# Optimization experiments

Hardware: AMD Instinct MI355X
Metric: run time of the kernel (lower is better)

The kernel has to match this reference:

```python
import jax, jax.numpy as jnp
import numpy as np

B, S, H, NH = 2, 2048, 1024, 16
HD = H // NH  # 64
EPS = 1e-5


def setup_inputs() -> dict:
    key = jax.random.key(0)
    ks = jax.random.split(key, 4)
    return {
        "hidden_states": jax.random.normal(ks[0], (B, S, H), dtype=jnp.float32),
        "W_attn": jax.random.normal(ks[1], (H, 3 * H), dtype=jnp.float32) * (1.0 / np.sqrt(H)),
        "b_attn": jnp.zeros((3 * H,), dtype=jnp.float32),
        "W_proj": jax.random.normal(ks[2], (H, H), dtype=jnp.float32) * (1.0 / np.sqrt(H)),
        "b_proj": jnp.zeros((H,), dtype=jnp.float32),
        "q_gamma": jnp.ones((HD,), dtype=jnp.float32),
        "q_beta": jnp.zeros((HD,), dtype=jnp.float32),
        "k_gamma": jnp.ones((HD,), dtype=jnp.float32),
        "k_beta": jnp.zeros((HD,), dtype=jnp.float32),
    }


def _layernorm(x, gamma, beta):
    mu = jnp.mean(x, axis=-1, keepdims=True)
    var = jnp.mean(jnp.square(x - mu), axis=-1, keepdims=True)
    return (x - mu) * jax.lax.rsqrt(var + EPS) * gamma + beta


def reference(hidden_states, W_attn, b_attn, W_proj, b_proj, q_gamma, q_beta, k_gamma, k_beta):
    b, s, h = hidden_states.shape
    qkv = hidden_states @ W_attn + b_attn  # [B,S,3H]
    q, k, v = jnp.split(qkv, 3, axis=-1)
    # [B,S,H] -> [B,NH,S,HD]
    def to_heads(t):
        return t.reshape(b, s, NH, HD).transpose(0, 2, 1, 3)
    q, k, v = to_heads(q), to_heads(k), to_heads(v)
    # QK LayerNorm over head_dim
    q = _layernorm(q, q_gamma, q_beta)
    k = _layernorm(k, k_gamma, k_beta)
    scale = HD ** (-0.5)
    scores = jnp.einsum("bhqd,bhkd->bhqk", q, k) * scale
    causal = jnp.tril(jnp.ones((s, s), dtype=bool))
    mask_value = jnp.finfo(scores.dtype).min
    scores = jnp.where(causal, scores, mask_value)
    attn = jax.nn.softmax(scores.astype(jnp.float32), axis=-1).astype(q.dtype)
    out = jnp.einsum("bhqk,bhkd->bhqd", attn, v)
    out = out.transpose(0, 2, 1, 3).reshape(b, s, h)
    out = out @ W_proj + b_proj
    return out
```

## Files before the change

### kernel.cpp

```cpp
#include <hip/hip_runtime.h>
#include <hip/hip_bf16.h>

typedef __bf16 bf16x8 __attribute__((ext_vector_type(8)));
typedef float f32x4 __attribute__((ext_vector_type(4)));

#define EPS 1e-5f
#define QSCALE 0.18033688011112042f

__device__ __forceinline__ unsigned short f2bf(float f) {
  union { float f; unsigned int i; } c; c.f = f;
  unsigned int r = c.i + 0x7FFFu + ((c.i >> 16) & 1u);
  return (unsigned short)(r >> 16);
}
__device__ __forceinline__ unsigned short f2bf_t(float f) {
  union { float f; unsigned int i; } c; c.f = f;
  return (unsigned short)(c.i >> 16);
}

__device__ __forceinline__ void glds16(const void* g, void* l) {
  __builtin_amdgcn_global_load_lds(
      (const __attribute__((address_space(1))) unsigned int*)g,
      (__attribute__((address_space(3))) unsigned int*)l, 16, 0, 0);
}

__device__ __forceinline__ void transpose_tile(
    const float* __restrict__ in, unsigned short* __restrict__ out,
    int R, int C, int ct0, int rt0, unsigned short* S )
{
  const int t = threadIdx.x;
  const int r = t >> 2, c4 = (t & 3) * 16;
  {
    long base = (long)(rt0 + r) * C + ct0 + c4;
    float4 a = *(const float4*)&in[base];
    float4 b = *(const float4*)&in[base + 4];
    float4 c = *(const float4*)&in[base + 8];
    float4 d = *(const float4*)&in[base + 12];
    unsigned short v[16] = {f2bf(a.x), f2bf(a.y), f2bf(a.z), f2bf(a.w),
                            f2bf(b.x), f2bf(b.y), f2bf(b.z), f2bf(b.w),
                            f2bf(c.x), f2bf(c.y), f2bf(c.z), f2bf(c.w),
                            f2bf(d.x), f2bf(d.y), f2bf(d.z), f2bf(d.w)};
    *(uint4*)&S[r * 72 + c4]     = *(uint4*)&v[0];
    *(uint4*)&S[r * 72 + c4 + 8] = *(uint4*)&v[8];
  }
  __syncthreads();
  unsigned short tmp[16];
#pragma unroll
  for (int j = 0; j < 16; j++) tmp[j] = S[(c4 + j) * 72 + r];
  *(uint4*)&out[(long)(ct0 + r) * R + rt0 + c4]     = *(uint4*)&tmp[0];
  *(uint4*)&out[(long)(ct0 + r) * R + rt0 + c4 + 8] = *(uint4*)&tmp[8];
}

__global__ __launch_bounds__(256) void prep_kernel(
    const float* __restrict__ Wa, const float* __restrict__ Wp,
    const float* __restrict__ X,
    unsigned short* __restrict__ WaT, unsigned short* __restrict__ WpT,
    unsigned short* __restrict__ Xbf)
{
  __shared__ __align__(16) unsigned short S[64 * 72];
  const int id = blockIdx.x;
  if (id < 768) {
    transpose_tile(Wa, WaT, 1024, 3072, (id % 48) * 64, (id / 48) * 64, S);
  } else if (id < 1024) {
    const int i2 = id - 768;
    transpose_tile(Wp, WpT, 1024, 1024, (i2 % 16) * 64, (i2 / 16) * 64, S);
  } else {
    long i = ((long)(id - 1024) * 256 + threadIdx.x) * 16;
    float4 a = *(const float4*)&X[i];
    float4 b = *(const float4*)&X[i + 4];
    float4 c = *(const float4*)&X[i + 8];
    float4 d = *(const float4*)&X[i + 12];
    unsigned short v[16] = {f2bf(a.x), f2bf(a.y), f2bf(a.z), f2bf(a.w),
                            f2bf(b.x), f2bf(b.y), f2bf(b.z), f2bf(b.w),
                            f2bf(c.x), f2bf(c.y), f2bf(c.z), f2bf(c.w),
                            f2bf(d.x), f2bf(d.y), f2bf(d.z), f2bf(d.w)};
    *(uint4*)&Xbf[i]     = *(uint4*)&v[0];
    *(uint4*)&Xbf[i + 8] = *(uint4*)&v[8];
  }
}

__global__ __launch_bounds__(256) void qkvt_kernel(
    const float* __restrict__ Xf,
    const unsigned short* __restrict__ Xbf, int use_xbf,
    const unsigned short* __restrict__ WT,
    const float* __restrict__ bias,
    const float* __restrict__ qg, const float* __restrict__ qb,
    const float* __restrict__ kg, const float* __restrict__ kb,
    unsigned short* __restrict__ Qws, unsigned short* __restrict__ Kws,
    unsigned short* __restrict__ Vt)
{
  __shared__ __align__(16) unsigned short As[2][128 * 32];
  __shared__ __align__(16) unsigned short Bs[2][128 * 32];

  const int tid = threadIdx.x;
  const int w = tid >> 6, lane = tid & 63, quad = lane >> 4, l15 = lane & 15;
  const int mh = w & 1, nh = w >> 1;
  const int id = blockIdx.x;
  const int grow = lane >> 2, gcol = (lane & 3) * 8;

  if (id < 512) {
    const int n0 = (id & 15) * 128, m0 = (id >> 4) * 128;

    f32x4 acc[4][4];
#pragma unroll
    for (int i = 0; i < 4; i++)
#pragma unroll
      for (int j = 0; j < 4; j++) acc[i][j] = (f32x4){0.f, 0.f, 0.f, 0.f};

    if (use_xbf) {
      const long ga = (long)(m0 + w * 32 + grow) * 1024 + gcol;
      const long gb = (long)(n0 + w * 32 + grow) * 1024 + gcol;
#define STAGE_QK(bf, kk) do { \
        glds16(&Xbf[ga + (kk)],             &As[bf][(w * 32) * 32]); \
        glds16(&Xbf[ga + (kk) + 16 * 1024], &As[bf][(w * 32 + 16) * 32]); \
        glds16(&WT[gb + (kk)],              &Bs[bf][(w * 32) * 32]); \
        glds16(&WT[gb + (kk) + 16 * 1024],  &Bs[bf][(w * 32 + 16) * 32]); \
      } while (0)
      STAGE_QK(0, 0);
      __syncthreads();
      int buf = 0;
      for (int kt = 0; kt < 1024; kt += 32) {
        if (kt + 32 < 1024) STAGE_QK(buf ^ 1, kt + 32);
        bf16x8 af[4], bfr[4];
#pragma unroll
        for (int mq = 0; mq < 4; mq++)
          af[mq] = *(const bf16x8*)&As[buf][(mh * 64 + mq * 16 + l15) * 32 + quad * 8];
#pragma unroll
        for (int nq = 0; nq < 4; nq++)
          bfr[nq] = *(const bf16x8*)&Bs[buf][(nh * 64 + nq * 16 + l15) * 32 + quad * 8];
#pragma unroll
        for (int mq = 0; mq < 4; mq++)
#pragma unroll
          for (int nq = 0; nq < 4; nq++)
            acc[mq][nq] = __builtin_amdgcn_mfma_f32_16x16x32_bf16(af[mq], bfr[nq], acc[mq][nq], 0, 0, 0);
        __syncthreads();
        buf ^= 1;
      }
#undef STAGE_QK
    } else {
      const int sr2 = tid >> 1, sh2 = (tid & 1) * 16;
      {
        long xo = (long)(m0 + sr2) * 1024 + sh2;
        float4 a0 = *(const float4*)&Xf[xo];
        float4 a1 = *(const float4*)&Xf[xo + 4];
        float4 a2 = *(const float4*)&Xf[xo + 8];
        float4 a3 = *(const float4*)&Xf[xo + 12];
        unsigned short v[16] = {f2bf(a0.x), f2bf(a0.y), f2bf(a0.z), f2bf(a0.w),
                                f2bf(a1.x), f2bf(a1.y), f2bf(a1.z), f2bf(a1.w),
                                f2bf(a2.x), f2bf(a2.y), f2bf(a2.z), f2bf(a2.w),
                                f2bf(a3.x), f2bf(a3.y), f2bf(a3.z), f2bf(a3.w)};
        *(uint4*)&As[0][sr2 * 32 + sh2]     = *(uint4*)&v[0];
        *(uint4*)&As[0][sr2 * 32 + sh2 + 8] = *(uint4*)&v[8];
        long wo = (long)(n0 + sr2) * 1024 + sh2;
        *(uint4*)&Bs[0][sr2 * 32 + sh2]     = *(const uint4*)&WT[wo];
        *(uint4*)&Bs[0][sr2 * 32 + sh2 + 8] = *(const uint4*)&WT[wo + 8];
      }
      __syncthreads();

      int buf = 0;
      for (int kt = 0; kt < 1024; kt += 32) {
        const int nbuf = buf ^ 1;
        const bool pf = (kt + 32) < 1024;
        uint4 wv0, wv1;
        float4 a0, a1, a2, a3;
        if (pf) {
          long xo = (long)(m0 + sr2) * 1024 + kt + 32 + sh2;
          a0 = *(const float4*)&Xf[xo];
          a1 = *(const float4*)&Xf[xo + 4];
          a2 = *(const float4*)&Xf[xo + 8];
          a3 = *(const float4*)&Xf[xo + 12];
          long wo = (long)(n0 + sr2) * 1024 + kt + 32 + sh2;
          wv0 = *(const uint4*)&WT[wo];
          wv1 = *(const uint4*)&WT[wo + 8];
        }

        bf16x8 af[4], bfr[4];
#pragma unroll
        for (int mq = 0; mq < 4; mq++)
          af[mq] = *(const bf16x8*)&As[buf][(mh * 64 + mq * 16 + l15) * 32 + quad * 8];
#pragma unroll
        for (int nq = 0; nq < 4; nq++)
          bfr[nq] = *(const bf16x8*)&Bs[buf][(nh * 64 + nq * 16 + l15) * 32 + quad * 8];
#pragma unroll
        for (int mq = 0; mq < 4; mq++)
#pragma unroll
          for (int nq = 0; nq < 4; nq++)
            acc[mq][nq] = __builtin_amdgcn_mfma_f32_16x16x32_bf16(af[mq], bfr[nq], acc[mq][nq], 0, 0, 0);

        if (pf) {
          unsigned short v[16] = {f2bf(a0.x), f2bf(a0.y), f2bf(a0.z), f2bf(a0.w),
                                  f2bf(a1.x), f2bf(a1.y), f2bf(a1.z), f2bf(a1.w),
                                  f2bf(a2.x), f2bf(a2.y), f2bf(a2.z), f2bf(a2.w),
                                  f2bf(a3.x), f2bf(a3.y), f2bf(a3.z), f2bf(a3.w)};
          *(uint4*)&As[nbuf][sr2 * 32 + sh2]     = *(uint4*)&v[0];
          *(uint4*)&As[nbuf][sr2 * 32 + sh2 + 8] = *(uint4*)&v[8];
          *(uint4*)&Bs[nbuf][sr2 * 32 + sh2]     = wv0;
          *(uint4*)&Bs[nbuf][sr2 * 32 + sh2 + 8] = wv1;
        }
        __syncthreads();
        buf = nbuf;
      }
    }

#pragma unroll
    for (int nq = 0; nq < 4; nq++) {
      float bv = bias[n0 + nh * 64 + nq * 16 + l15];
#pragma unroll
      for (int mq = 0; mq < 4; mq++)
#pragma unroll
        for (int rr = 0; rr < 4; rr++) acc[mq][nq][rr] += bv;
    }

    const int g = (n0 >> 6) + nh;
    const bool isQ = g < 16;
    {
      float gv[4], bev[4];
#pragma unroll
      for (int nq = 0; nq < 4; nq++) {
        int d = nq * 16 + l15;
        gv[nq]  = isQ ? qg[d] : kg[d];
        bev[nq] = isQ ? qb[d] : kb[d];
        if (isQ) { gv[nq] *= QSCALE; bev[nq] *= QSCALE; }
      }
#pragma unroll
      for (int mq = 0; mq < 4; mq++)
#pragma unroll
        for (int rr = 0; rr < 4; rr++) {
          float s  = acc[mq][0][rr] + acc[mq][1][rr] + acc[mq][2][rr] + acc[mq][3][rr];
          float s2 = acc[mq][0][rr]*acc[mq][0][rr] + acc[mq][1][rr]*acc[mq][1][rr]
                   + acc[mq][2][rr]*acc[mq][2][rr] + acc[mq][3][rr]*acc[mq][3][rr];
#pragma unroll
          for (int off = 1; off < 16; off <<= 1) {
            s  += __shfl_xor(s,  off, 64);
            s2 += __shfl_xor(s2, off, 64);
          }
          float mu   = s * (1.0f / 64.0f);
          float var  = fmaxf(s2 * (1.0f / 64.0f) - mu * mu, 0.f);
          float rstd = rsqrtf(var + EPS);
#pragma unroll
          for (int nq = 0; nq < 4; nq++)
            acc[mq][nq][rr] = (acc[mq][nq][rr] - mu) * rstd * gv[nq] + bev[nq];
        }
    }

    unsigned short* dst = isQ ? Qws : Kws;
    const int head = isQ ? g : g - 16;
#pragma unroll
    for (int mq = 0; mq < 4; mq++)
#pragma unroll
      for (int rr = 0; rr < 4; rr++) {
        int m = m0 + mh * 64 + mq * 16 + quad * 4 + rr;
        int b = m >> 11, s = m & 2047;
        long base = ((long)((b * 16 + head) * 2048 + s)) * 64;
#pragma unroll
        for (int nq = 0; nq < 4; nq++)
          dst[base + nq * 16 + l15] = f2bf(acc[mq][nq][rr]);
      }
  } else {
    const int id2 = id - 512;
    const int n0 = (id2 & 31) * 64, m0 = ((id2 >> 5) & 7) * 128, bz = id2 >> 8;
    const long xrow0 = (long)bz * 2048;
    const unsigned short* WvT = WT + 2048L * 1024;

    f32x4 acc[4][2];
#pragma unroll
    for (int i = 0; i < 4; i++)
#pragma unroll
      for (int j = 0; j < 2; j++) acc[i][j] = (f32x4){0.f, 0.f, 0.f, 0.f};

    if (use_xbf) {
      const long gva = (long)(m0 + w * 32 + grow) * 1024 + gcol;
      const long gvb = (xrow0 + n0 + w * 16 + grow) * 1024 + gcol;
#define STAGE_V(bf, kk) do { \
        glds16(&WvT[gva + (kk)],             &As[bf][(w * 32) * 32]); \
        glds16(&WvT[gva + (kk) + 16 * 1024], &As[bf][(w * 32 + 16) * 32]); \
        glds16(&Xbf[gvb + (kk)],             &Bs[bf][(w * 16) * 32]); \
      } while (0)
      STAGE_V(0, 0);
      __syncthreads();
      int buf = 0;
      for (int kt = 0; kt < 1024; kt += 32) {
        if (kt + 32 < 1024) STAGE_V(buf ^ 1, kt + 32);
        bf16x8 af[4], bfr[2];
#pragma unroll
        for (int mq = 0; mq < 4; mq++)
          af[mq] = *(const bf16x8*)&As[buf][(mh * 64 + mq * 16 + l15) * 32 + quad * 8];
#pragma unroll
        for (int nq = 0; nq < 2; nq++)
          bfr[nq] = *(const bf16x8*)&Bs[buf][(nh * 32 + nq * 16 + l15) * 32 + quad * 8];
#pragma unroll
        for (int mq = 0; mq < 4; mq++)
#pragma unroll
          for (int nq = 0; nq < 2; nq++)
            acc[mq][nq] = __builtin_amdgcn_mfma_f32_16x16x32_bf16(af[mq], bfr[nq], acc[mq][nq], 0, 0, 0);
        __syncthreads();
        buf ^= 1;
      }
#undef STAGE_V
    } else {
      const int srA = tid >> 1, shA = (tid & 1) * 16;
      const int srB = tid >> 2, shB = (tid & 3) * 8;
      {
        long wo = (long)(m0 + srA) * 1024 + shA;
        *(uint4*)&As[0][srA * 32 + shA]     = *(const uint4*)&WvT[wo];
        *(uint4*)&As[0][srA * 32 + shA + 8] = *(const uint4*)&WvT[wo + 8];
        long xo = (xrow0 + n0 + srB) * 1024 + shB;
        float4 a0 = *(const float4*)&Xf[xo];
        float4 a1 = *(const float4*)&Xf[xo + 4];
        unsigned short v[8] = {f2bf(a0.x), f2bf(a0.y), f2bf(a0.z), f2bf(a0.w),
                               f2bf(a1.x), f2bf(a1.y), f2bf(a1.z), f2bf(a1.w)};
        *(uint4*)&Bs[0][srB * 32 + shB] = *(uint4*)v;
      }
      __syncthreads();

      int buf = 0;
      for (int kt = 0; kt < 1024; kt += 32) {
        const int nbuf = buf ^ 1;
        const bool pf = (kt + 32) < 1024;
        uint4 wv0, wv1, xv0;
        float4 a0, a1;
        if (pf) {
          long wo = (long)(m0 + srA) * 1024 + kt + 32 + shA;
          wv0 = *(const uint4*)&WvT[wo];
          wv1 = *(const uint4*)&WvT[wo + 8];
          long xo = (xrow0 + n0 + srB) * 1024 + kt + 32 + shB;
          a0 = *(const float4*)&Xf[xo];
          a1 = *(const float4*)&Xf[xo + 4];
        }

        bf16x8 af[4], bfr[2];
#pragma unroll
        for (int mq = 0; mq < 4; mq++)
          af[mq] = *(const bf16x8*)&As[buf][(mh * 64 + mq * 16 + l15) * 32 + quad * 8];
#pragma unroll
        for (int nq = 0; nq < 2; nq++)
          bfr[nq] = *(const bf16x8*)&Bs[buf][(nh * 32 + nq * 16 + l15) * 32 + quad * 8];
#pragma unroll
        for (int mq = 0; mq < 4; mq++)
#pragma unroll
          for (int nq = 0; nq < 2; nq++)
            acc[mq][nq] = __builtin_amdgcn_mfma_f32_16x16x32_bf16(af[mq], bfr[nq], acc[mq][nq], 0, 0, 0);

        if (pf) {
          *(uint4*)&As[nbuf][srA * 32 + shA]     = wv0;
          *(uint4*)&As[nbuf][srA * 32 + shA + 8] = wv1;
          unsigned short v[8] = {f2bf(a0.x), f2bf(a0.y), f2bf(a0.z), f2bf(a0.w),
                                 f2bf(a1.x), f2bf(a1.y), f2bf(a1.z), f2bf(a1.w)};
          *(uint4*)&Bs[nbuf][srB * 32 + shB] = *(uint4*)v;
        }
        __syncthreads();
        buf = nbuf;
      }
    }

    const long outb = (long)bz * 2097152;
#pragma unroll
    for (int mq = 0; mq < 4; mq++)
#pragma unroll
      for (int rr = 0; rr < 4; rr++) {
        int m = m0 + mh * 64 + mq * 16 + quad * 4 + rr;
        float bv = bias[2048 + m];
#pragma unroll
        for (int nq = 0; nq < 2; nq++) {
          int n = n0 + nh * 32 + nq * 16 + l15;
          Vt[outb + (long)m * 2048 + n] = f2bf(acc[mq][nq][rr] + bv);
        }
      }
  }
}

__global__ __launch_bounds__(256) void attn_kernel(
    unsigned short* __restrict__ Qws,
    const unsigned short* __restrict__ Kws,
    const unsigned short* __restrict__ Vt)
{
  __shared__ __align__(16) unsigned short Ks[2][64 * 72];
  __shared__ __align__(16) unsigned short VTs[2][64 * 72];
  __shared__ __align__(16) unsigned short Ps[64 * 64];

  const int tid = threadIdx.x;
  const int w = tid >> 6, lane = tid & 63, quad = lane >> 4, l15 = lane & 15;
  const int id = blockIdx.x;
  const int bh = (id & 7) * 4 + ((id >> 3) & 3);
  const int x  = id >> 5;
  const long bhoff = (long)bh * 2048 * 64;
  const long bhv   = (long)bh * 131072;

  const int sr = tid >> 2, sc = (tid & 3) * 16;
  const int qsw = ((sr >> 2) & 3) << 4;
  const int sw = ((l15 >> 2) & 3) << 4;
  const int pc0 = (quad * 8) ^ sw;
  const int pc1 = (32 + quad * 8) ^ sw;

  bf16x8 ones;
  {
    union { unsigned short u[8]; bf16x8 v; } c;
#pragma unroll
    for (int i = 0; i < 8; i++) c.u[i] = 0x3F80u;
    ones = c.v;
  }

#pragma unroll
  for (int ph = 0; ph < 2; ph++) {
    const int qt = ph ? (31 - x) : x;
    const int qbase = qt * 64;
    const int jmax = qt + 1;

    if (ph) __syncthreads();

    *(uint4*)&Ps[sr * 64 + (sc ^ qsw)]       = *(const uint4*)&Qws[bhoff + (qbase + sr) * 64 + sc];
    *(uint4*)&Ps[sr * 64 + ((sc ^ qsw) + 8)] = *(const uint4*)&Qws[bhoff + (qbase + sr) * 64 + sc + 8];
    *(uint4*)&Ks[0][sr * 72 + sc]      = *(const uint4*)&Kws[bhoff + sr * 64 + sc];
    *(uint4*)&Ks[0][sr * 72 + sc + 8]  = *(const uint4*)&Kws[bhoff + sr * 64 + sc + 8];
    *(uint4*)&VTs[0][sr * 72 + sc]     = *(const uint4*)&Vt[bhv + sr * 2048 + sc];
    *(uint4*)&VTs[0][sr * 72 + sc + 8] = *(const uint4*)&Vt[bhv + sr * 2048 + sc + 8];
    __syncthreads();

    const bf16x8 qf0 = *(const bf16x8*)&Ps[(w * 16 + l15) * 64 + pc0];
    const bf16x8 qf1 = *(const bf16x8*)&Ps[(w * 16 + l15) * 64 + pc1];

    f32x4 o[4], osum;
#pragma unroll
    for (int i = 0; i < 4; i++) o[i] = (f32x4){0.f, 0.f, 0.f, 0.f};
    osum = (f32x4){0.f, 0.f, 0.f, 0.f};

    int cb = 0;
    for (int j = 0; j < jmax; j++) {
      const int kb = j * 64;
      const bool pf = (j + 1) < jmax;
      uint4 pk0, pk1, pv0, pv1;
      if (pf) {
        const int kb1 = kb + 64;
        pk0 = *(const uint4*)&Kws[bhoff + (kb1 + sr) * 64 + sc];
        pk1 = *(const uint4*)&Kws[bhoff + (kb1 + sr) * 64 + sc + 8];
        pv0 = *(const uint4*)&Vt[bhv + sr * 2048 + kb1 + sc];
        pv1 = *(const uint4*)&Vt[bhv + sr * 2048 + kb1 + sc + 8];
      }

      f32x4 sacc[4];
#pragma unroll
      for (int i = 0; i < 4; i++) sacc[i] = (f32x4){0.f, 0.f, 0.f, 0.f};
#pragma unroll
      for (int nt = 0; nt < 4; nt++) {
        bf16x8 kf0 = *(const bf16x8*)&Ks[cb][(nt * 16 + l15) * 72 + quad * 8];
        bf16x8 kf1 = *(const bf16x8*)&Ks[cb][(nt * 16 + l15) * 72 + 32 + quad * 8];
        sacc[nt] = __builtin_amdgcn_mfma_f32_16x16x32_bf16(qf0, kf0, sacc[nt], 0, 0, 0);
        sacc[nt] = __builtin_amdgcn_mfma_f32_16x16x32_bf16(qf1, kf1, sacc[nt], 0, 0, 0);
      }

      const bool domask = (j == qt);
#pragma unroll
      for (int nt = 0; nt < 4; nt++)
#pragma unroll
        for (int rr = 0; rr < 4; rr++) {
          float p = exp2f(sacc[nt][rr]);
          if (domask) {
            int kcol = kb + nt * 16 + l15;
            int qrow = qbase + w * 16 + quad * 4 + rr;
            if (kcol > qrow) p = 0.f;
          }
          sacc[nt][rr] = p;
        }

#pragma unroll
      for (int rr = 0; rr < 4; rr++)
#pragma unroll
        for (int nt = 0; nt < 4; nt++)
          Ps[(w * 16 + quad * 4 + rr) * 64 + (((nt ^ quad) & 3) * 16 + l15)]
              = f2bf_t(sacc[nt][rr]);

      bf16x8 pfr0 = *(const bf16x8*)&Ps[(w * 16 + l15) * 64 + pc0];
      bf16x8 pfr1 = *(const bf16x8*)&Ps[(w * 16 + l15) * 64 + pc1];

      osum = __builtin_amdgcn_mfma_f32_16x16x32_bf16(pfr0, ones, osum, 0, 0, 0);
      osum = __builtin_amdgcn_mfma_f32_16x16x32_bf16(pfr1, ones, osum, 0, 0, 0);
#pragma unroll
      for (int dt = 0; dt < 4; dt++) {
        bf16x8 vf0 = *(const bf16x8*)&VTs[cb][(dt * 16 + l15) * 72 + quad * 8];
        bf16x8 vf1 = *(const bf16x8*)&VTs[cb][(dt * 16 + l15) * 72 + 32 + quad * 8];
        o[dt] = __builtin_amdgcn_mfma_f32_16x16x32_bf16(pfr0, vf0, o[dt], 0, 0, 0);
        o[dt] = __builtin_amdgcn_mfma_f32_16x16x32_bf16(pfr1, vf1, o[dt], 0, 0, 0);
      }

      if (pf) {
        const int nb = cb ^ 1;
        *(uint4*)&Ks[nb][sr * 72 + sc]      = pk0;
        *(uint4*)&Ks[nb][sr * 72 + sc + 8]  = pk1;
        *(uint4*)&VTs[nb][sr * 72 + sc]     = pv0;
        *(uint4*)&VTs[nb][sr * 72 + sc + 8] = pv1;
        __syncthreads();
        cb = nb;
      }
    }

#pragma unroll
    for (int rr = 0; rr < 4; rr++) {
      float inv = 1.0f / osum[rr];
      int row = qbase + w * 16 + quad * 4 + rr;
      long base = bhoff + (long)row * 64;
#pragma unroll
      for (int dt = 0; dt < 4; dt++)
        Qws[base + dt * 16 + l15] = f2bf(o[dt][rr] * inv);
    }
  }
}

__global__ __launch_bounds__(256) void proj_kernel(
    const unsigned short* __restrict__ AQ,
    const unsigned short* __restrict__ WT,
    const float* __restrict__ bias,
    float* __restrict__ Out)
{
  __shared__ __align__(16) unsigned short As[2][128 * 32];
  __shared__ __align__(16) unsigned short Bs[2][64 * 32];

  const int tid = threadIdx.x;
  const int w = tid >> 6, lane = tid & 63, quad = lane >> 4, l15 = lane & 15;
  const int mh = w & 1, nh = w >> 1;
  const int n0 = blockIdx.x * 64, m0 = blockIdx.y * 128;

  f32x4 acc[4][2];
#pragma unroll
  for (int i = 0; i < 4; i++)
#pragma unroll
    for (int j = 0; j < 2; j++) acc[i][j] = (f32x4){0.f, 0.f, 0.f, 0.f};

  const int srA = tid >> 1, shA = (tid & 1) * 16;
  const int srB = tid >> 2, shB = (tid & 3) * 8;
  const int m = m0 + srA, b = m >> 11, s = m & 2047;

  {
    const int h = shA >> 6, d = shA & 63;
    long ao = ((long)((b * 16 + h) * 2048 + s)) * 64 + d;
    *(uint4*)&As[0][srA * 32 + shA]     = *(const uint4*)&AQ[ao];
    *(uint4*)&As[0][srA * 32 + shA + 8] = *(const uint4*)&AQ[ao + 8];
    long wo = (long)(n0 + srB) * 1024 + shB;
    *(uint4*)&Bs[0][srB * 32 + shB] = *(const uint4*)&WT[wo];
  }
  __syncthreads();

  int buf = 0;
  for (int kt = 0; kt < 1024; kt += 32) {
    const int nbuf = buf ^ 1;
    const bool pf = (kt + 32) < 1024;
    uint4 av0, av1, wv0;
    if (pf) {
      const int k = kt + 32 + shA, h = k >> 6, d = k & 63;
      long ao = ((long)((b * 16 + h) * 2048 + s)) * 64 + d;
      av0 = *(const uint4*)&AQ[ao];
      av1 = *(const uint4*)&AQ[ao + 8];
      long wo = (long)(n0 + srB) * 1024 + kt + 32 + shB;
      wv0 = *(const uint4*)&WT[wo];
    }

    bf16x8 af[4], bfr[2];
#pragma unroll
    for (int mq = 0; mq < 4; mq++)
      af[mq] = *(const bf16x8*)&As[buf][(mh * 64 + mq * 16 + l15) * 32 + quad * 8];
#pragma unroll
    for (int nq = 0; nq < 2; nq++)
      bfr[nq] = *(const bf16x8*)&Bs[buf][(nh * 32 + nq * 16 + l15) * 32 + quad * 8];
#pragma unroll
    for (int mq = 0; mq < 4; mq++)
#pragma unroll
      for (int nq = 0; nq < 2; nq++)
        acc[mq][nq] = __builtin_amdgcn_mfma_f32_16x16x32_bf16(af[mq], bfr[nq], acc[mq][nq], 0, 0, 0);

    if (pf) {
      *(uint4*)&As[nbuf][srA * 32 + shA]     = av0;
      *(uint4*)&As[nbuf][srA * 32 + shA + 8] = av1;
      *(uint4*)&Bs[nbuf][srB * 32 + shB]     = wv0;
    }
    __syncthreads();
    buf = nbuf;
  }

#pragma unroll
  for (int nq = 0; nq < 2; nq++) {
    int n = n0 + nh * 32 + nq * 16 + l15;
    float bv = bias[n];
#pragma unroll
    for (int mq = 0; mq < 4; mq++)
#pragma unroll
      for (int rr = 0; rr < 4; rr++) {
        int mm = m0 + mh * 64 + mq * 16 + quad * 4 + rr;
        Out[(long)mm * 1024 + n] = acc[mq][nq][rr] + bv;
      }
  }
}

extern "C" void kernel_launch(void* const* d_in, const int* in_sizes, int n_in,
                              void* d_out, int out_size, void* d_ws, size_t ws_size,
                              hipStream_t stream) {
  const float* X  = (const float*)d_in[0];
  const float* Wa = (const float*)d_in[1];
  const float* ba = (const float*)d_in[2];
  const float* Wp = (const float*)d_in[3];
  const float* bp = (const float*)d_in[4];
  const float* qg = (const float*)d_in[5];
  const float* qb = (const float*)d_in[6];
  const float* kg = (const float*)d_in[7];
  const float* kb = (const float*)d_in[8];

  const long per = 2L * 16 * 2048 * 64;
  unsigned short* ws  = (unsigned short*)d_ws;
  unsigned short* Qws = ws;
  unsigned short* Kws = Qws + per;
  unsigned short* Vt  = Kws + per;

  const bool big = ws_size >= (size_t)(5L * per * 2);
  unsigned short *Xbf, *WaT, *WpT;
  if (big) {
    Xbf = Vt + per;
    WaT = Xbf + per;
    WpT = WaT + 3072L * 1024;
  } else {
    Xbf = Qws;
    WaT = Vt + per;
    WpT = WaT + 3072L * 1024;
  }

  prep_kernel<<<big ? 2048 : 1024, 256, 0, stream>>>(Wa, Wp, X, WaT, WpT, Xbf);
  qkvt_kernel<<<1024, 256, 0, stream>>>(X, Xbf, big ? 1 : 0, WaT, ba,
                                        qg, qb, kg, kb, Qws, Kws, Vt);
  attn_kernel<<<512, 256, 0, stream>>>(Qws, Kws, Vt);
  proj_kernel<<<dim3(16, 32), 256, 0, stream>>>(Qws, WpT, bp, (float*)d_out);
}
```

Before: 207.9 us.

## Run both causal query tiles concurrently in a 512-thread attention block

The attention kernel now launches 512 threads per block and splits them into two 4-wave groups. Each group handles one of the paired query tiles (short and long) at the same time, where before the block processed them one after the other. The K/V tile loads are shared: one group fetches K and the other fetches V. This halves redundant global loads and per-block serial latency. In exchange, the short-tile group sits idle at barriers once its causal range ends, and the larger block may lower occupancy.

```diff
diff --git a/kernel.cpp b/kernel.cpp
--- a/kernel.cpp
+++ b/kernel.cpp
@@ -316,7 +316,7 @@
       for (int kt = 0; kt < 1024; kt += 32) {
         const int nbuf = buf ^ 1;
         const bool pf = (kt + 32) < 1024;
-        uint4 wv0, wv1, xv0;
+        uint4 wv0, wv1;
         float4 a0, a1;
         if (pf) {
           long wo = (long)(m0 + srA) * 1024 + kt + 32 + shA;
@@ -368,24 +368,32 @@
   }
 }
 
-__global__ __launch_bounds__(256) void attn_kernel(
+__global__ __launch_bounds__(512) void attn_kernel(
     unsigned short* __restrict__ Qws,
     const unsigned short* __restrict__ Kws,
     const unsigned short* __restrict__ Vt)
 {
   __shared__ __align__(16) unsigned short Ks[2][64 * 72];
   __shared__ __align__(16) unsigned short VTs[2][64 * 72];
-  __shared__ __align__(16) unsigned short Ps[64 * 64];
+  __shared__ __align__(16) unsigned short Ps[2][64 * 64];
 
   const int tid = threadIdx.x;
   const int w = tid >> 6, lane = tid & 63, quad = lane >> 4, l15 = lane & 15;
+  const int g = w >> 2, wq = w & 3;
   const int id = blockIdx.x;
   const int bh = (id & 7) * 4 + ((id >> 3) & 3);
-  const int x  = id >> 5;
+  const int i5 = id >> 5;
+  const int x  = (i5 < 8) ? i5 : 23 - i5;
   const long bhoff = (long)bh * 2048 * 64;
   const long bhv   = (long)bh * 131072;
 
-  const int sr = tid >> 2, sc = (tid & 3) * 16;
+  const int qt_long = 31 - x;
+  const int myqt  = g ? x : qt_long;
+  const int qbase = myqt * 64;
+  const int jsteps = qt_long + 1;
+
+  const int t2 = tid & 255;
+  const int sr = t2 >> 2, sc = (t2 & 3) * 16;
   const int qsw = ((sr >> 2) & 3) << 4;
   const int sw = ((l15 >> 2) & 3) << 4;
   const int pc0 = (quad * 8) ^ sw;
@@ -399,43 +407,42 @@
     ones = c.v;
   }
 
-#pragma unroll
-  for (int ph = 0; ph < 2; ph++) {
-    const int qt = ph ? (31 - x) : x;
-    const int qbase = qt * 64;
-    const int jmax = qt + 1;
-
-    if (ph) __syncthreads();
-
-    *(uint4*)&Ps[sr * 64 + (sc ^ qsw)]       = *(const uint4*)&Qws[bhoff + (qbase + sr) * 64 + sc];
-    *(uint4*)&Ps[sr * 64 + ((sc ^ qsw) + 8)] = *(const uint4*)&Qws[bhoff + (qbase + sr) * 64 + sc + 8];
+  *(uint4*)&Ps[g][sr * 64 + (sc ^ qsw)]       = *(const uint4*)&Qws[bhoff + (qbase + sr) * 64 + sc];
+  *(uint4*)&Ps[g][sr * 64 + ((sc ^ qsw) + 8)] = *(const uint4*)&Qws[bhoff + (qbase + sr) * 64 + sc + 8];
+  if (g == 0) {
     *(uint4*)&Ks[0][sr * 72 + sc]      = *(const uint4*)&Kws[bhoff + sr * 64 + sc];
     *(uint4*)&Ks[0][sr * 72 + sc + 8]  = *(const uint4*)&Kws[bhoff + sr * 64 + sc + 8];
+  } else {
     *(uint4*)&VTs[0][sr * 72 + sc]     = *(const uint4*)&Vt[bhv + sr * 2048 + sc];
     *(uint4*)&VTs[0][sr * 72 + sc + 8] = *(const uint4*)&Vt[bhv + sr * 2048 + sc + 8];
-    __syncthreads();
-
-    const bf16x8 qf0 = *(const bf16x8*)&Ps[(w * 16 + l15) * 64 + pc0];
-    const bf16x8 qf1 = *(const bf16x8*)&Ps[(w * 16 + l15) * 64 + pc1];
-
-    f32x4 o[4], osum;
-#pragma unroll
-    for (int i = 0; i < 4; i++) o[i] = (f32x4){0.f, 0.f, 0.f, 0.f};
-    osum = (f32x4){0.f, 0.f, 0.f, 0.f};
-
-    int cb = 0;
-    for (int j = 0; j < jmax; j++) {
-      const int kb = j * 64;
-      const bool pf = (j + 1) < jmax;
-      uint4 pk0, pk1, pv0, pv1;
-      if (pf) {
-        const int kb1 = kb + 64;
-        pk0 = *(const uint4*)&Kws[bhoff + (kb1 + sr) * 64 + sc];
-        pk1 = *(const uint4*)&Kws[bhoff + (kb1 + sr) * 64 + sc + 8];
-        pv0 = *(const uint4*)&Vt[bhv + sr * 2048 + kb1 + sc];
-        pv1 = *(const uint4*)&Vt[bhv + sr * 2048 + kb1 + sc + 8];
-      }
-
+  }
+  __syncthreads();
+
+  const bf16x8 qf0 = *(const bf16x8*)&Ps[g][(wq * 16 + l15) * 64 + pc0];
+  const bf16x8 qf1 = *(const bf16x8*)&Ps[g][(wq * 16 + l15) * 64 + pc1];
+
+  f32x4 o[4], osum;
+#pragma unroll
+  for (int i = 0; i < 4; i++) o[i] = (f32x4){0.f, 0.f, 0.f, 0.f};
+  osum = (f32x4){0.f, 0.f, 0.f, 0.f};
+
+  int cb = 0;
+  for (int j = 0; j < jsteps; j++) {
+    const int kb = j * 64;
+    const bool pf = (j + 1) < jsteps;
+    uint4 p0, p1;
+    if (pf) {
+      const int kb1 = kb + 64;
+      if (g == 0) {
+        p0 = *(const uint4*)&Kws[bhoff + (kb1 + sr) * 64 + sc];
+        p1 = *(const uint4*)&Kws[bhoff + (kb1 + sr) * 64 + sc + 8];
+      } else {
+        p0 = *(const uint4*)&Vt[bhv + sr * 2048 + kb1 + sc];
+        p1 = *(const uint4*)&Vt[bhv + sr * 2048 + kb1 + sc + 8];
+      }
+    }
+
+    if (j <= myqt) {
       f32x4 sacc[4];
 #pragma unroll
       for (int i = 0; i < 4; i++) sacc[i] = (f32x4){0.f, 0.f, 0.f, 0.f};
@@ -447,7 +454,7 @@
         sacc[nt] = __builtin_amdgcn_mfma_f32_16x16x32_bf16(qf1, kf1, sacc[nt], 0, 0, 0);
       }
 
-      const bool domask = (j == qt);
+      const bool domask = (j == myqt);
 #pragma unroll
       for (int nt = 0; nt < 4; nt++)
 #pragma unroll
@@ -455,7 +462,7 @@
           float p = exp2f(sacc[nt][rr]);
           if (domask) {
             int kcol = kb + nt * 16 + l15;
-            int qrow = qbase + w * 16 + quad * 4 + rr;
+            int qrow = qbase + wq * 16 + quad * 4 + rr;
             if (kcol > qrow) p = 0.f;
           }
           sacc[nt][rr] = p;
@@ -465,11 +472,11 @@
       for (int rr = 0; rr < 4; rr++)
 #pragma unroll
         for (int nt = 0; nt < 4; nt++)
-          Ps[(w * 16 + quad * 4 + rr) * 64 + (((nt ^ quad) & 3) * 16 + l15)]
+          Ps[g][(wq * 16 + quad * 4 + rr) * 64 + (((nt ^ quad) & 3) * 16 + l15)]
               = f2bf_t(sacc[nt][rr]);
 
-      bf16x8 pfr0 = *(const bf16x8*)&Ps[(w * 16 + l15) * 64 + pc0];
-      bf16x8 pfr1 = *(const bf16x8*)&Ps[(w * 16 + l15) * 64 + pc1];
+      bf16x8 pfr0 = *(const bf16x8*)&Ps[g][(wq * 16 + l15) * 64 + pc0];
+      bf16x8 pfr1 = *(const bf16x8*)&Ps[g][(wq * 16 + l15) * 64 + pc1];
 
       osum = __builtin_amdgcn_mfma_f32_16x16x32_bf16(pfr0, ones, osum, 0, 0, 0);
       osum = __builtin_amdgcn_mfma_f32_16x16x32_bf16(pfr1, ones, osum, 0, 0, 0);
@@ -480,27 +487,30 @@
         o[dt] = __builtin_amdgcn_mfma_f32_16x16x32_bf16(pfr0, vf0, o[dt], 0, 0, 0);
         o[dt] = __builtin_amdgcn_mfma_f32_16x16x32_bf16(pfr1, vf1, o[dt], 0, 0, 0);
       }
-
-      if (pf) {
-        const int nb = cb ^ 1;
-        *(uint4*)&Ks[nb][sr * 72 + sc]      = pk0;
-        *(uint4*)&Ks[nb][sr * 72 + sc + 8]  = pk1;
-        *(uint4*)&VTs[nb][sr * 72 + sc]     = pv0;
-        *(uint4*)&VTs[nb][sr * 72 + sc + 8] = pv1;
-        __syncthreads();
-        cb = nb;
-      }
-    }
-
-#pragma unroll
-    for (int rr = 0; rr < 4; rr++) {
-      float inv = 1.0f / osum[rr];
-      int row = qbase + w * 16 + quad * 4 + rr;
-      long base = bhoff + (long)row * 64;
-#pragma unroll
-      for (int dt = 0; dt < 4; dt++)
-        Qws[base + dt * 16 + l15] = f2bf(o[dt][rr] * inv);
-    }
+    }
+
+    if (pf) {
+      const int nb = cb ^ 1;
+      if (g == 0) {
+        *(uint4*)&Ks[nb][sr * 72 + sc]      = p0;
+        *(uint4*)&Ks[nb][sr * 72 + sc + 8]  = p1;
+      } else {
+        *(uint4*)&VTs[nb][sr * 72 + sc]     = p0;
+        *(uint4*)&VTs[nb][sr * 72 + sc + 8] = p1;
+      }
+      __syncthreads();
+      cb = nb;
+    }
+  }
+
+#pragma unroll
+  for (int rr = 0; rr < 4; rr++) {
+    float inv = 1.0f / osum[rr];
+    int row = qbase + wq * 16 + quad * 4 + rr;
+    long base = bhoff + (long)row * 64;
+#pragma unroll
+    for (int dt = 0; dt < 4; dt++)
+      Qws[base + dt * 16 + l15] = f2bf(o[dt][rr] * inv);
   }
 }
 
@@ -622,6 +632,6 @@
   prep_kernel<<<big ? 2048 : 1024, 256, 0, stream>>>(Wa, Wp, X, WaT, WpT, Xbf);
   qkvt_kernel<<<1024, 256, 0, stream>>>(X, Xbf, big ? 1 : 0, WaT, ba,
                                         qg, qb, kg, kb, Qws, Kws, Vt);
-  attn_kernel<<<512, 256, 0, stream>>>(Qws, Kws, Vt);
+  attn_kernel<<<512, 512, 0, stream>>>(Qws, Kws, Vt);
   proj_kernel<<<dim3(16, 32), 256, 0, stream>>>(Qws, WpT, bp, (float*)d_out);
 }
```

Result: no change. 205.9 us (-1.0%).
